# Optimization experiments

Hardware: AMD Instinct MI355X
Metric: run time of the kernel (lower is better)

## Reference

```python
import jax, jax.numpy as jnp
import numpy as np

N_NODES = 100000
N_EDGES = 1600000
IN_CH = 64
OUT_CH = 64


def setup_inputs() -> dict:
    key = jax.random.key(0)
    k1, k2, k3, k4 = jax.random.split(key, 4)
    x = jax.random.normal(k1, (N_NODES, IN_CH), dtype=jnp.float32)
    edge_index = jax.random.randint(k2, (2, N_EDGES), 0, N_NODES, dtype=jnp.int64)
    # Linear(2*in, out) and Linear(out, out); stored as [in, out] for x @ W
    W1 = jax.random.normal(k3, (2 * IN_CH, OUT_CH), dtype=jnp.float32) * (1.0 / np.sqrt(2 * IN_CH))
    b1 = jnp.zeros((OUT_CH,), dtype=jnp.float32)
    W2 = jax.random.normal(k4, (OUT_CH, OUT_CH), dtype=jnp.float32) * (1.0 / np.sqrt(OUT_CH))
    b2 = jnp.zeros((OUT_CH,), dtype=jnp.float32)
    return {"x": x, "edge_index": edge_index, "W1": W1, "b1": b1, "W2": W2, "b2": b2}


def reference(x, edge_index, W1, b1, W2, b2):
    # EdgeConv: for each edge (j -> i), m_e = MLP(concat([x_i, x_j - x_i]));
    # node output = max over incoming edges (empty nodes -> 0, matching scatter-max fill).
    src = edge_index[0]  # j
    dst = edge_index[1]  # i
    xi = x[dst]                      # [E, C]
    xj = x[src]                      # [E, C]
    h = jnp.concatenate([xi, xj - xi], axis=-1)      # [E, 2C]
    h = jax.nn.relu(h @ W1 + b1)                     # [E, OUT]
    h = jax.nn.relu(h @ W2 + b2)                     # [E, OUT]
    out = jax.ops.segment_max(h, dst, num_segments=x.shape[0])  # [N, OUT]
    return jnp.where(jnp.isfinite(out), out, jnp.zeros_like(out))
```

## Files before the change

kernel.cpp:

```cpp
#include <hip/hip_runtime.h>
#include <hip/hip_bf16.h>

typedef __bf16 bf16x8 __attribute__((ext_vector_type(8)));
typedef __bf16 bf16x4 __attribute__((ext_vector_type(4)));
typedef float f32x4 __attribute__((ext_vector_type(4)));

#define EB 256
#define NSCAN 1024

#define OFF_COUNTS 0
#define OFF_STARTS 100000
#define OFF_BSUM   200016
#define OFF_CSR    200160
#define WAB_DW 6144

__device__ __forceinline__ unsigned short f2bf(float v) {
    unsigned int u = __float_as_uint(v);
    return (unsigned short)((u + 0x7fffu + ((u >> 16) & 1u)) >> 16);
}

__device__ __forceinline__ bf16x8 pack8(float4 a, float4 b) {
    bf16x8 r;
    r[0] = (__bf16)a.x; r[1] = (__bf16)a.y; r[2] = (__bf16)a.z; r[3] = (__bf16)a.w;
    r[4] = (__bf16)b.x; r[5] = (__bf16)b.y; r[6] = (__bf16)b.z; r[7] = (__bf16)b.w;
    return r;
}

__global__ void prep_hist_kernel(const float* __restrict__ W1,
                                 const float* __restrict__ W2,
                                 unsigned short* __restrict__ wab,
                                 const int* __restrict__ ei,
                                 int* __restrict__ counts,
                                 int* __restrict__ slot, int E) {
    int b = blockIdx.x;
    if (b < 48) {
        int t = b * 256 + threadIdx.x;
        if (t < 4096) {
            int c = t >> 6, k = t & 63;
            wab[t] = f2bf(W1[k * 64 + c] - W1[(64 + k) * 64 + c]);
        } else if (t < 8192) {
            int i = t - 4096;
            int c = i >> 6, k = i & 63;
            wab[t] = f2bf(W1[(64 + k) * 64 + c]);
        } else if (t < 12288) {
            int i = t - 8192;
            int o = i >> 6, c = i & 63;
            wab[t] = f2bf(W2[c * 64 + o]);
        }
        return;
    }
    int t = (b - 48) * 256 + threadIdx.x;
    int i = t * 4;
    if (i + 3 < E) {
        int4 d = *(const int4*)(ei + E + i);
        int4 s;
        s.x = atomicAdd(&counts[d.x], 1);
        s.y = atomicAdd(&counts[d.y], 1);
        s.z = atomicAdd(&counts[d.z], 1);
        s.w = atomicAdd(&counts[d.w], 1);
        *(int4*)(slot + i) = s;
    } else {
        for (int j = 0; j < 4 && i + j < E; ++j)
            slot[i + j] = atomicAdd(&counts[ei[E + i + j]], 1);
    }
}

__global__ __launch_bounds__(256, 4)
void ab_kernel(const float* __restrict__ x,
               const unsigned short* __restrict__ wab,
               const float* __restrict__ b1,
               unsigned short* __restrict__ Abf,
               unsigned short* __restrict__ Bbf, int N) {
    const int lane = threadIdx.x & 63;
    const int w    = threadIdx.x >> 6;
    const int ln   = lane & 15;
    const int rg   = lane >> 4;
    const int n    = blockIdx.x * 64 + w * 16 + ln;
    const int nc   = min(n, N - 1);

    const float* xr = x + (long)nc * 64;
    float4 f0 = *(const float4*)(xr + rg * 8),      f1 = *(const float4*)(xr + rg * 8 + 4);
    float4 f2 = *(const float4*)(xr + 32 + rg * 8), f3 = *(const float4*)(xr + 32 + rg * 8 + 4);
    bf16x8 xk[2];
    xk[0] = pack8(f0, f1);
    xk[1] = pack8(f2, f3);

    const bf16x8* wAv = (const bf16x8*)wab;
    const bf16x8* wBv = (const bf16x8*)(wab + 4096);

    f32x4 accA[4], accB[4];
    #pragma unroll
    for (int ct = 0; ct < 4; ++ct) {
        accA[ct] = (f32x4){0.f, 0.f, 0.f, 0.f};
        accB[ct] = (f32x4){0.f, 0.f, 0.f, 0.f};
    }
    #pragma unroll
    for (int kt = 0; kt < 2; ++kt) {
        #pragma unroll
        for (int ct = 0; ct < 4; ++ct) {
            accA[ct] = __builtin_amdgcn_mfma_f32_16x16x32_bf16(
                wAv[(ct * 16 + ln) * 8 + kt * 4 + rg], xk[kt], accA[ct], 0, 0, 0);
            accB[ct] = __builtin_amdgcn_mfma_f32_16x16x32_bf16(
                wBv[(ct * 16 + ln) * 8 + kt * 4 + rg], xk[kt], accB[ct], 0, 0, 0);
        }
    }
    if (n < N) {
        #pragma unroll
        for (int ct = 0; ct < 4; ++ct) {
            const int c0 = ct * 16 + rg * 4;
            float4 bv = *(const float4*)(b1 + c0);
            bf16x4 av, bvv;
            av[0] = (__bf16)(accA[ct][0] + bv.x);
            av[1] = (__bf16)(accA[ct][1] + bv.y);
            av[2] = (__bf16)(accA[ct][2] + bv.z);
            av[3] = (__bf16)(accA[ct][3] + bv.w);
            bvv[0] = (__bf16)accB[ct][0];
            bvv[1] = (__bf16)accB[ct][1];
            bvv[2] = (__bf16)accB[ct][2];
            bvv[3] = (__bf16)accB[ct][3];
            *(bf16x4*)(Abf + (long)n * 64 + c0) = av;
            *(bf16x4*)(Bbf + (long)n * 64 + c0) = bvv;
        }
    }
}

__global__ void scanA_kernel(const int* __restrict__ counts, int* __restrict__ bsum, int N) {
    int b = blockIdx.x, t = threadIdx.x;
    int base = b * NSCAN + t * 4;
    int s = 0;
    #pragma unroll
    for (int q = 0; q < 4; ++q)
        if (base + q < N) s += counts[base + q];
    #pragma unroll
    for (int off = 1; off < 64; off <<= 1) s += __shfl_xor(s, off);
    __shared__ int wsum[4];
    if ((t & 63) == 0) wsum[t >> 6] = s;
    __syncthreads();
    if (t == 0) bsum[b] = wsum[0] + wsum[1] + wsum[2] + wsum[3];
}

__global__ void scanB_kernel(int* __restrict__ bsum, int* __restrict__ starts, int nb, int N, int E) {
    int lane = threadIdx.x;
    int v0 = (lane < nb) ? bsum[lane] : 0;
    int v1 = (64 + lane < nb) ? bsum[64 + lane] : 0;
    int s = v0;
    #pragma unroll
    for (int off = 1; off < 64; off <<= 1) {
        int n = __shfl_up(s, off);
        if (lane >= off) s += n;
    }
    int total0 = __shfl(s, 63);
    int s1 = v1;
    #pragma unroll
    for (int off = 1; off < 64; off <<= 1) {
        int n = __shfl_up(s1, off);
        if (lane >= off) s1 += n;
    }
    if (lane < nb) bsum[lane] = s - v0;
    if (64 + lane < nb) bsum[64 + lane] = total0 + s1 - v1;
    if (lane == 0) starts[N] = E;
}

__global__ void scanC_kernel(const int* __restrict__ counts, const int* __restrict__ bsum,
                             int* __restrict__ starts, float* __restrict__ out, int N) {
    int b = blockIdx.x, t = threadIdx.x;
    int lane = t & 63, w = t >> 6;
    int base = b * NSCAN + t * 4;
    int c[4];
    #pragma unroll
    for (int q = 0; q < 4; ++q)
        c[q] = (base + q < N) ? counts[base + q] : 0;
    int tot = c[0] + c[1] + c[2] + c[3];
    int inc = tot;
    #pragma unroll
    for (int off = 1; off < 64; off <<= 1) {
        int n = __shfl_up(inc, off);
        if (lane >= off) inc += n;
    }
    int excl = inc - tot;
    __shared__ int wtot[4];
    if (lane == 63) wtot[w] = inc;
    __syncthreads();
    int woff = 0;
    for (int i = 0; i < w; ++i) woff += wtot[i];
    int run = bsum[b] + woff + excl;
    #pragma unroll
    for (int q = 0; q < 4; ++q) {
        if (base + q < N) {
            starts[base + q] = run;
            if (c[q] == 0) {
                f32x4 z = (f32x4){0.f, 0.f, 0.f, 0.f};
                float* op = out + (long)(base + q) * 64;
                #pragma unroll
                for (int r = 0; r < 16; ++r) *(f32x4*)(op + r * 4) = z;
            }
            run += c[q];
        }
    }
}

__global__ void scatter_kernel(const int* __restrict__ ei, const int* __restrict__ starts,
                               const int* __restrict__ slot, int2* __restrict__ csr, int E) {
    int t = blockIdx.x * blockDim.x + threadIdx.x;
    if (t < E) {
        int s = ei[t], d = ei[E + t];
        int p = starts[d] + slot[t];
        csr[p] = make_int2(s, d);
    }
}

__global__ __launch_bounds__(256)
void edgeconv_kernel(const unsigned short* __restrict__ Abf,
                     const unsigned short* __restrict__ Bbf,
                     const int2* __restrict__ csr,
                     const int* __restrict__ starts,
                     const float* __restrict__ b2,
                     const unsigned short* __restrict__ wab,
                     float* __restrict__ out,
                     int E) {
    __shared__ __align__(16) unsigned char sB[EB * 128];

    const int tid  = threadIdx.x;
    const int lane = tid & 63;
    const int w    = tid >> 6;
    const int ln   = lane & 15;
    const int rg   = lane >> 4;
    const int p0   = blockIdx.x * EB;
    const int p1   = min(p0 + EB, E);

    const bf16x8* w2v = (const bf16x8*)(wab + 8192);

    bf16x8 fr[4][2];
    #pragma unroll
    for (int eti = 0; eti < 4; ++eti) {
        const int p = p0 + (w * 4 + eti) * 16 + ln;
        int2 sd = (p < E) ? csr[p] : make_int2(0, 0);
        const unsigned short* Ai = Abf + (long)sd.y * 64;
        const unsigned short* Bj = Bbf + (long)sd.x * 64;
        bf16x8 a0 = *(const bf16x8*)(Ai + rg * 8);
        bf16x8 a1 = *(const bf16x8*)(Ai + 32 + rg * 8);
        bf16x8 q0 = *(const bf16x8*)(Bj + rg * 8);
        bf16x8 q1 = *(const bf16x8*)(Bj + 32 + rg * 8);
        #pragma unroll
        for (int j = 0; j < 8; ++j) {
            fr[eti][0][j] = (__bf16)fmaxf((float)a0[j] + (float)q0[j], 0.f);
            fr[eti][1][j] = (__bf16)fmaxf((float)a1[j] + (float)q1[j], 0.f);
        }
    }

    f32x4 acc2[4][4];
    #pragma unroll
    for (int eti = 0; eti < 4; ++eti)
        #pragma unroll
        for (int ot = 0; ot < 4; ++ot)
            acc2[eti][ot] = (f32x4){0.f, 0.f, 0.f, 0.f};

    #pragma unroll
    for (int kt = 0; kt < 2; ++kt) {
        #pragma unroll
        for (int ot = 0; ot < 4; ++ot) {
            bf16x8 wf = w2v[(ot * 16 + ln) * 8 + kt * 4 + rg];
            #pragma unroll
            for (int eti = 0; eti < 4; ++eti)
                acc2[eti][ot] = __builtin_amdgcn_mfma_f32_16x16x32_bf16(
                    wf, fr[eti][kt], acc2[eti][ot], 0, 0, 0);
        }
    }

    #pragma unroll
    for (int eti = 0; eti < 4; ++eti) {
        const int e = (w * 4 + eti) * 16 + ln;
        unsigned char* rowp = sB + e * 128;
        const unsigned int swz = (unsigned int)(e & 7) << 4;
        #pragma unroll
        for (int ot = 0; ot < 4; ++ot) {
            const int c0 = ot * 16 + rg * 4;
            float4 bv = *(const float4*)(b2 + c0);
            bf16x4 hv;
            hv[0] = (__bf16)fmaxf(acc2[eti][ot][0] + bv.x, 0.f);
            hv[1] = (__bf16)fmaxf(acc2[eti][ot][1] + bv.y, 0.f);
            hv[2] = (__bf16)fmaxf(acc2[eti][ot][2] + bv.z, 0.f);
            hv[3] = (__bf16)fmaxf(acc2[eti][ot][3] + bv.w, 0.f);
            *(bf16x4*)(rowp + (((unsigned)(c0 * 2)) ^ swz)) = hv;
        }
    }

    __syncthreads();

    {
        const int dfirst = csr[p0].y;
        const int dlast  = csr[p1 - 1].y;
        const int c = lane;
        for (int d = dfirst + w; d <= dlast; d += 4) {
            const int s0 = starts[d], s1 = starts[d + 1];
            const int lo = max(s0, p0), hi = min(s1, p1);
            if (lo >= hi) continue;
            unsigned int m0 = 0, m1 = 0;
            int p = lo;
            for (; p + 1 < hi; p += 2) {
                const int e0 = p - p0, e1 = e0 + 1;
                unsigned int v0 = *(const unsigned short*)(sB + e0 * 128 +
                                    (((unsigned)(c * 2)) ^ ((unsigned)(e0 & 7) << 4)));
                unsigned int v1 = *(const unsigned short*)(sB + e1 * 128 +
                                    (((unsigned)(c * 2)) ^ ((unsigned)(e1 & 7) << 4)));
                m0 = max(m0, v0);
                m1 = max(m1, v1);
            }
            if (p < hi) {
                const int e0 = p - p0;
                unsigned int v0 = *(const unsigned short*)(sB + e0 * 128 +
                                    (((unsigned)(c * 2)) ^ ((unsigned)(e0 & 7) << 4)));
                m0 = max(m0, v0);
            }
            float m = __uint_as_float(max(m0, m1) << 16);
            if (s0 >= p0 && s1 <= p1)
                out[(long)d * 64 + c] = m;
            else
                atomicMax((int*)out + (long)d * 64 + c, __float_as_int(m));
        }
    }
}

extern "C" void kernel_launch(void* const* d_in, const int* in_sizes, int n_in,
                              void* d_out, int out_size, void* d_ws, size_t ws_size,
                              hipStream_t stream) {
    const float* x  = (const float*)d_in[0];
    const int*   ei = (const int*)d_in[1];
    const float* W1 = (const float*)d_in[2];
    const float* b1 = (const float*)d_in[3];
    const float* W2 = (const float*)d_in[4];
    const float* b2 = (const float*)d_in[5];
    float* out = (float*)d_out;

    const int E = in_sizes[1] / 2;
    const int N = in_sizes[0] / 64;

    int* wsI = (int*)d_ws;
    int* counts  = wsI + OFF_COUNTS;
    int* starts  = wsI + OFF_STARTS;
    int* bsum    = wsI + OFF_BSUM;
    int2* csr    = (int2*)(wsI + OFF_CSR);
    unsigned short* wab = (unsigned short*)(wsI + OFF_CSR + 2 * E);
    unsigned short* Abf = (unsigned short*)(wsI + OFF_CSR + 2 * E + WAB_DW);
    unsigned short* Bbf = Abf + (long)N * 64;
    int* slot = (int*)Abf;

    hipMemsetAsync(counts, 0, (size_t)N * sizeof(int), stream);

    const int nbH = (E / 4 + 255) / 256 + 1;
    prep_hist_kernel<<<48 + nbH, 256, 0, stream>>>(W1, W2, wab, ei, counts, slot, E);

    const int nb2 = (N + NSCAN - 1) / NSCAN;
    scanA_kernel<<<nb2, 256, 0, stream>>>(counts, bsum, N);
    scanB_kernel<<<1, 64, 0, stream>>>(bsum, starts, nb2, N, E);
    scanC_kernel<<<nb2, 256, 0, stream>>>(counts, bsum, starts, out, N);

    const int nbE = (E + 255) / 256;
    scatter_kernel<<<nbE, 256, 0, stream>>>(ei, starts, slot, csr, E);

    const int nbAB = (N + 63) / 64;
    ab_kernel<<<nbAB, 256, 0, stream>>>(x, wab, b1, Abf, Bbf, N);

    const int nb = (E + EB - 1) / EB;
    edgeconv_kernel<<<nb, 256, 0, stream>>>(Abf, Bbf, csr, starts, b2, wab, out, E);
}
```

Baseline: 230.1 us.

## Fuse three-pass scan into single-pass lookback, vectorize scatter, enlarge edge blocks

Replaces the three scan kernels with one kernel in which each block publishes its total and spin-waits on all earlier blocks' flags to build its prefix. This cuts two launches and a serial single-block pass. The scatter kernel now handles four edges per thread using int4 loads. The edgeconv kernel processes 512 edges per block with 512 threads, and the segment-max loop stride changes to 8 waves. The spin-wait assumes earlier blocks are scheduled first, which holds for about 98 blocks but is not guaranteed. The larger LDS tile and block may reduce occupancy.

```diff
diff --git a/kernel.cpp b/kernel.cpp
--- a/kernel.cpp
+++ b/kernel.cpp
@@ -5,13 +5,14 @@
 typedef __bf16 bf16x4 __attribute__((ext_vector_type(4)));
 typedef float f32x4 __attribute__((ext_vector_type(4)));
 
-#define EB 256
+#define EB 512
 #define NSCAN 1024
 
 #define OFF_COUNTS 0
 #define OFF_STARTS 100000
-#define OFF_BSUM   200016
-#define OFF_CSR    200160
+#define OFF_VAL    200016
+#define OFF_STATE  200144
+#define OFF_CSR    200448
 #define WAB_DW 6144
 
 __device__ __forceinline__ unsigned short f2bf(float v) {
@@ -29,11 +30,13 @@
 __global__ void prep_hist_kernel(const float* __restrict__ W1,
                                  const float* __restrict__ W2,
                                  unsigned short* __restrict__ wab,
+                                 int* __restrict__ state,
                                  const int* __restrict__ ei,
                                  int* __restrict__ counts,
                                  int* __restrict__ slot, int E) {
     int b = blockIdx.x;
     if (b < 48) {
+        if (b == 0 && threadIdx.x < 128) state[threadIdx.x] = 0;
         int t = b * 256 + threadIdx.x;
         if (t < 4096) {
             int c = t >> 6, k = t & 63;
@@ -62,6 +65,90 @@
     } else {
         for (int j = 0; j < 4 && i + j < E; ++j)
             slot[i + j] = atomicAdd(&counts[ei[E + i + j]], 1);
+    }
+}
+
+__global__ void scan_fused_kernel(const int* __restrict__ counts,
+                                  int* __restrict__ val, int* __restrict__ state,
+                                  int* __restrict__ starts, float* __restrict__ out,
+                                  int N, int E, int nb) {
+    int b = blockIdx.x, t = threadIdx.x;
+    int lane = t & 63, w = t >> 6;
+    int base = b * NSCAN + t * 4;
+    int c[4];
+    #pragma unroll
+    for (int q = 0; q < 4; ++q)
+        c[q] = (base + q < N) ? counts[base + q] : 0;
+    int tot = c[0] + c[1] + c[2] + c[3];
+
+    int s = tot;
+    #pragma unroll
+    for (int off = 1; off < 64; off <<= 1) s += __shfl_xor(s, off);
+    __shared__ int wsum[4];
+    if (lane == 0) wsum[w] = s;
+    __syncthreads();
+
+    __shared__ int sPrefix;
+    if (t == 0) {
+        int blockTot = wsum[0] + wsum[1] + wsum[2] + wsum[3];
+        val[b] = blockTot;
+        __threadfence();
+        atomicExch(&state[b], 1);
+        int pre = 0;
+        for (int i = 0; i < b; ++i) {
+            while (atomicAdd(&state[i], 0) == 0) { }
+            pre += atomicAdd(&val[i], 0);
+        }
+        sPrefix = pre;
+        if (b == nb - 1) starts[N] = E;
+    }
+
+    int inc = tot;
+    #pragma unroll
+    for (int off = 1; off < 64; off <<= 1) {
+        int n = __shfl_up(inc, off);
+        if (lane >= off) inc += n;
+    }
+    int excl = inc - tot;
+    __shared__ int wtot[4];
+    if (lane == 63) wtot[w] = inc;
+    __syncthreads();
+
+    int woff = 0;
+    for (int i = 0; i < w; ++i) woff += wtot[i];
+    int run = sPrefix + woff + excl;
+    #pragma unroll
+    for (int q = 0; q < 4; ++q) {
+        if (base + q < N) {
+            starts[base + q] = run;
+            if (c[q] == 0) {
+                f32x4 z = (f32x4){0.f, 0.f, 0.f, 0.f};
+                float* op = out + (long)(base + q) * 64;
+                #pragma unroll
+                for (int r = 0; r < 16; ++r) *(f32x4*)(op + r * 4) = z;
+            }
+            run += c[q];
+        }
+    }
+}
+
+__global__ void scatter_kernel(const int* __restrict__ ei, const int* __restrict__ starts,
+                               const int* __restrict__ slot, int2* __restrict__ csr, int E) {
+    int t = blockIdx.x * blockDim.x + threadIdx.x;
+    int i = t * 4;
+    if (i + 3 < E) {
+        int4 s4 = *(const int4*)(ei + i);
+        int4 d4 = *(const int4*)(ei + E + i);
+        int4 sl = *(const int4*)(slot + i);
+        csr[starts[d4.x] + sl.x] = make_int2(s4.x, d4.x);
+        csr[starts[d4.y] + sl.y] = make_int2(s4.y, d4.y);
+        csr[starts[d4.z] + sl.z] = make_int2(s4.z, d4.z);
+        csr[starts[d4.w] + sl.w] = make_int2(s4.w, d4.w);
+    } else {
+        for (int j = 0; j < 4 && i + j < E; ++j) {
+            int sE = ei[i + j], dE = ei[E + i + j];
+            csr[starts[dE] + slot[i + j]] = make_int2(sE, dE);
+        }
     }
 }
 
@@ -124,92 +211,7 @@
     }
 }
 
-__global__ void scanA_kernel(const int* __restrict__ counts, int* __restrict__ bsum, int N) {
-    int b = blockIdx.x, t = threadIdx.x;
-    int base = b * NSCAN + t * 4;
-    int s = 0;
-    #pragma unroll
-    for (int q = 0; q < 4; ++q)
-        if (base + q < N) s += counts[base + q];
-    #pragma unroll
-    for (int off = 1; off < 64; off <<= 1) s += __shfl_xor(s, off);
-    __shared__ int wsum[4];
-    if ((t & 63) == 0) wsum[t >> 6] = s;
-    __syncthreads();
-    if (t == 0) bsum[b] = wsum[0] + wsum[1] + wsum[2] + wsum[3];
-}
-
-__global__ void scanB_kernel(int* __restrict__ bsum, int* __restrict__ starts, int nb, int N, int E) {
-    int lane = threadIdx.x;
-    int v0 = (lane < nb) ? bsum[lane] : 0;
-    int v1 = (64 + lane < nb) ? bsum[64 + lane] : 0;
-    int s = v0;
-    #pragma unroll
-    for (int off = 1; off < 64; off <<= 1) {
-        int n = __shfl_up(s, off);
-        if (lane >= off) s += n;
-    }
-    int total0 = __shfl(s, 63);
-    int s1 = v1;
-    #pragma unroll
-    for (int off = 1; off < 64; off <<= 1) {
-        int n = __shfl_up(s1, off);
-        if (lane >= off) s1 += n;
-    }
-    if (lane < nb) bsum[lane] = s - v0;
-    if (64 + lane < nb) bsum[64 + lane] = total0 + s1 - v1;
-    if (lane == 0) starts[N] = E;
-}
-
-__global__ void scanC_kernel(const int* __restrict__ counts, const int* __restrict__ bsum,
-                             int* __restrict__ starts, float* __restrict__ out, int N) {
-    int b = blockIdx.x, t = threadIdx.x;
-    int lane = t & 63, w = t >> 6;
-    int base = b * NSCAN + t * 4;
-    int c[4];
-    #pragma unroll
-    for (int q = 0; q < 4; ++q)
-        c[q] = (base + q < N) ? counts[base + q] : 0;
-    int tot = c[0] + c[1] + c[2] + c[3];
-    int inc = tot;
-    #pragma unroll
-    for (int off = 1; off < 64; off <<= 1) {
-        int n = __shfl_up(inc, off);
-        if (lane >= off) inc += n;
-    }
-    int excl = inc - tot;
-    __shared__ int wtot[4];
-    if (lane == 63) wtot[w] = inc;
-    __syncthreads();
-    int woff = 0;
-    for (int i = 0; i < w; ++i) woff += wtot[i];
-    int run = bsum[b] + woff + excl;
-    #pragma unroll
-    for (int q = 0; q < 4; ++q) {
-        if (base + q < N) {
-            starts[base + q] = run;
-            if (c[q] == 0) {
-                f32x4 z = (f32x4){0.f, 0.f, 0.f, 0.f};
-                float* op = out + (long)(base + q) * 64;
-                #pragma unroll
-                for (int r = 0; r < 16; ++r) *(f32x4*)(op + r * 4) = z;
-            }
-            run += c[q];
-        }
-    }
-}
-
-__global__ void scatter_kernel(const int* __restrict__ ei, const int* __restrict__ starts,
-                               const int* __restrict__ slot, int2* __restrict__ csr, int E) {
-    int t = blockIdx.x * blockDim.x + threadIdx.x;
-    if (t < E) {
-        int s = ei[t], d = ei[E + t];
-        int p = starts[d] + slot[t];
-        csr[p] = make_int2(s, d);
-    }
-}
-
-__global__ __launch_bounds__(256)
+__global__ __launch_bounds__(512)
 void edgeconv_kernel(const unsigned short* __restrict__ Abf,
                      const unsigned short* __restrict__ Bbf,
                      const int2* __restrict__ csr,
@@ -291,7 +293,7 @@
         const int dfirst = csr[p0].y;
         const int dlast  = csr[p1 - 1].y;
         const int c = lane;
-        for (int d = dfirst + w; d <= dlast; d += 4) {
+        for (int d = dfirst + w; d <= dlast; d += 8) {
             const int s0 = starts[d], s1 = starts[d + 1];
             const int lo = max(s0, p0), hi = min(s1, p1);
             if (lo >= hi) continue;
@@ -338,7 +340,8 @@
     int* wsI = (int*)d_ws;
     int* counts  = wsI + OFF_COUNTS;
     int* starts  = wsI + OFF_STARTS;
-    int* bsum    = wsI + OFF_BSUM;
+    int* val     = wsI + OFF_VAL;
+    int* state   = wsI + OFF_STATE;
     int2* csr    = (int2*)(wsI + OFF_CSR);
     unsigned short* wab = (unsigned short*)(wsI + OFF_CSR + 2 * E);
     unsigned short* Abf = (unsigned short*)(wsI + OFF_CSR + 2 * E + WAB_DW);
@@ -348,19 +351,17 @@
     hipMemsetAsync(counts, 0, (size_t)N * sizeof(int), stream);
 
     const int nbH = (E / 4 + 255) / 256 + 1;
-    prep_hist_kernel<<<48 + nbH, 256, 0, stream>>>(W1, W2, wab, ei, counts, slot, E);
+    prep_hist_kernel<<<48 + nbH, 256, 0, stream>>>(W1, W2, wab, state, ei, counts, slot, E);
 
     const int nb2 = (N + NSCAN - 1) / NSCAN;
-    scanA_kernel<<<nb2, 256, 0, stream>>>(counts, bsum, N);
-    scanB_kernel<<<1, 64, 0, stream>>>(bsum, starts, nb2, N, E);
-    scanC_kernel<<<nb2, 256, 0, stream>>>(counts, bsum, starts, out, N);
-
-    const int nbE = (E + 255) / 256;
-    scatter_kernel<<<nbE, 256, 0, stream>>>(ei, starts, slot, csr, E);
+    scan_fused_kernel<<<nb2, 256, 0, stream>>>(counts, val, state, starts, out, N, E, nb2);
+
+    const int nbS = (E / 4 + 255) / 256 + 1;
+    scatter_kernel<<<nbS, 256, 0, stream>>>(ei, starts, slot, csr, E);
 
     const int nbAB = (N + 63) / 64;
     ab_kernel<<<nbAB, 256, 0, stream>>>(x, wab, b1, Abf, Bbf, N);
 
     const int nb = (E + EB - 1) / EB;
-    edgeconv_kernel<<<nb, 256, 0, stream>>>(Abf, Bbf, csr, starts, b2, wab, out, E);
-}
+    edgeconv_kernel<<<nb, 512, 0, stream>>>(Abf, Bbf, csr, starts, b2, wab, out, E);
+}
```

Result: slower. 289.2 us (+25.7%).
